# Optimization experiments

Hardware: AMD Instinct MI355X
Metric: run time of the kernel (lower is better)

## Reference

```python
import jax, jax.numpy as jnp
import numpy as np

HEAD_SIZE = 64
N_EMBD = 128
B, T = 16, 2048


def setup_inputs() -> dict:
    key = jax.random.key(0)
    ks = jax.random.split(key, 7)
    s = 1.0 / np.sqrt(N_EMBD)
    return {
        "x": jax.random.normal(ks[0], (B, T, N_EMBD), dtype=jnp.float32),
        "Wk": jax.random.normal(ks[1], (N_EMBD, HEAD_SIZE), dtype=jnp.float32) * s,
        "bk": jax.random.normal(ks[2], (HEAD_SIZE,), dtype=jnp.float32) * s,
        "Wq": jax.random.normal(ks[3], (N_EMBD, HEAD_SIZE), dtype=jnp.float32) * s,
        "bq": jax.random.normal(ks[4], (HEAD_SIZE,), dtype=jnp.float32) * s,
        "Wv": jax.random.normal(ks[5], (N_EMBD, HEAD_SIZE), dtype=jnp.float32) * s,
        "bv": jax.random.normal(ks[6], (HEAD_SIZE,), dtype=jnp.float32) * s,
    }


def reference(x, Wk, bk, Wq, bq, Wv, bv):
    # x: [B, T, C]; single-head causal attention (dropout in eval mode = identity)
    Tdim = x.shape[1]
    k = x @ Wk + bk  # [B, T, H]
    q = x @ Wq + bq  # [B, T, H]
    v = x @ Wv + bv  # [B, T, H]
    scale = jnp.asarray(k.shape[-1], x.dtype) ** -0.5
    wei = jnp.einsum("bth,bsh->bts", q, k) * scale  # [B, T, T]
    causal = jnp.tril(jnp.ones((Tdim, Tdim), dtype=bool))
    wei = jnp.where(causal, wei, -jnp.inf)
    wei = jax.nn.softmax(wei, axis=-1)
    out = jnp.einsum("bts,bsh->bth", wei, v)  # [B, T, H]
    return out
```

## Files before the change

kernel.cpp:

```cpp
#include <hip/hip_runtime.h>
#include <hip/hip_bf16.h>
#include <math.h>

#define HS 64
#define NE 128
#define TSEQ 2048

typedef short s8v __attribute__((ext_vector_type(8)));
typedef float f4v __attribute__((ext_vector_type(4)));

__device__ __forceinline__ unsigned short f2bf(float f) {
    unsigned int u = __float_as_uint(f);
    u += 0x7FFFu + ((u >> 16) & 1u);
    return (unsigned short)(u >> 16);
}

__device__ __forceinline__ unsigned int pkbf(float a, float b) {
    union { __hip_bfloat162 h; unsigned int u; } cv;
    cv.h = __float22bfloat162_rn(make_float2(a, b));
    return cv.u;
}

__device__ __forceinline__ s8v mk_s8v(unsigned int a, unsigned int b,
                                      unsigned int c, unsigned int d) {
    union { unsigned int u[4]; s8v v; } cv;
    cv.u[0] = a; cv.u[1] = b; cv.u[2] = c; cv.u[3] = d;
    return cv.v;
}

__device__ __forceinline__ float fexp2(float x) {
    float r;
    asm("v_exp_f32 %0, %1" : "=v"(r) : "v"(x));
    return r;
}

__device__ __forceinline__ void glds16(const unsigned short* g, unsigned short* l) {
    __builtin_amdgcn_global_load_lds(
        (const __attribute__((address_space(1))) unsigned int*)g,
        (__attribute__((address_space(3))) unsigned int*)l,
        16, 0, 0);
}

__global__ __launch_bounds__(256) void wconv(
    const float* __restrict__ Wq, const float* __restrict__ Wk,
    const float* __restrict__ Wv, unsigned short* __restrict__ wt)
{
    const int o0 = (blockIdx.x * 256 + threadIdx.x) * 2;
    const int mat = o0 >> 13;
    const int n = (o0 >> 7) & 63;
    const int k = o0 & 127;
    const float* W = (mat == 0) ? Wq : (mat == 1) ? Wk : Wv;
    const float s = (mat == 0) ? 0.18033688f : 1.0f;
    unsigned int lo = f2bf(W[k * HS + n] * s);
    unsigned int hi = f2bf(W[(k + 1) * HS + n] * s);
    *(unsigned int*)(wt + o0) = lo | (hi << 16);
}

__global__ __launch_bounds__(256) void qkv(
    const float* __restrict__ x, const unsigned short* __restrict__ wt,
    const float* __restrict__ bq, const float* __restrict__ bk,
    const float* __restrict__ bv,
    unsigned short* __restrict__ qo, unsigned short* __restrict__ ko,
    unsigned short* __restrict__ vt)
{
    __shared__ __align__(16) unsigned short Ws[192 * 136];

    const int tid = threadIdx.x;
    const int w = tid >> 6;
    const int lane = tid & 63;
    const int quad = lane >> 4;
    const int li = lane & 15;
    const size_t blk0 = (size_t)blockIdx.x * 64;
    const size_t row0w = blk0 + (size_t)w * 16;

#pragma unroll
    for (int p = 0; p < 12; ++p) {
        const int idx = p * 256 + tid;
        const int n = idx >> 4;
        const int c = idx & 15;
        s8v d = *(const s8v*)(wt + idx * 8);
        *(s8v*)&Ws[n * 136 + c * 8] = d;
    }

    s8v a[4];
    const float* xr = x + (row0w + li) * NE + quad * 8;
#pragma unroll
    for (int ks = 0; ks < 4; ++ks) {
        float4 f0 = *(const float4*)(xr + ks * 32);
        float4 f1 = *(const float4*)(xr + ks * 32 + 4);
        a[ks] = mk_s8v(pkbf(f0.x, f0.y), pkbf(f0.z, f0.w),
                       pkbf(f1.x, f1.y), pkbf(f1.z, f1.w));
    }

    __syncthreads();

    f4v acc[12];
#pragma unroll
    for (int nt = 0; nt < 12; ++nt) acc[nt] = (f4v){0.f, 0.f, 0.f, 0.f};

#pragma unroll
    for (int nt = 0; nt < 12; ++nt) {
        const unsigned short* wr = &Ws[(nt * 16 + li) * 136 + quad * 8];
#pragma unroll
        for (int ks = 0; ks < 4; ++ks) {
            s8v bfr = *(const s8v*)(wr + ks * 32);
            acc[nt] = __builtin_amdgcn_mfma_f32_16x16x32_bf16(a[ks], bfr, acc[nt], 0, 0, 0);
        }
    }

    const size_t bidx = row0w >> 11;
    const size_t trow0 = row0w & 2047;
#pragma unroll
    for (int nt = 0; nt < 4; ++nt) {
        const float bias = bv[nt * 16 + li];
        unsigned int lo = pkbf(acc[nt + 8][0] + bias, acc[nt + 8][1] + bias);
        unsigned int hi = pkbf(acc[nt + 8][2] + bias, acc[nt + 8][3] + bias);
        *(uint2*)(vt + (bidx * HS + nt * 16 + li) * TSEQ + trow0 + quad * 4) =
            make_uint2(lo, hi);
    }

    __syncthreads();

    float* Qt = (float*)Ws;
    float* Kt = Qt + 64 * 68;
    const float sq = 0.18033688f;
    const int lrow0 = w * 16 + quad * 4;
#pragma unroll
    for (int nt = 0; nt < 4; ++nt) {
        const int col = nt * 16 + li;
        const float bq_ = bq[col] * sq;
        const float bk_ = bk[col];
#pragma unroll
        for (int r = 0; r < 4; ++r) {
            Qt[(lrow0 + r) * 68 + col] = acc[nt][r] + bq_;
            Kt[(lrow0 + r) * 68 + col] = acc[nt + 4][r] + bk_;
        }
    }

    __syncthreads();

    const int row = tid >> 2;
    const int seg = tid & 3;
    {
        const float* src = &Qt[row * 68 + seg * 16];
        float4 f0 = *(const float4*)src;
        float4 f1 = *(const float4*)(src + 4);
        float4 f2 = *(const float4*)(src + 8);
        float4 f3 = *(const float4*)(src + 12);
        s8v d0 = mk_s8v(pkbf(f0.x, f0.y), pkbf(f0.z, f0.w), pkbf(f1.x, f1.y), pkbf(f1.z, f1.w));
        s8v d1 = mk_s8v(pkbf(f2.x, f2.y), pkbf(f2.z, f2.w), pkbf(f3.x, f3.y), pkbf(f3.z, f3.w));
        unsigned short* dst = qo + (blk0 + row) * HS + seg * 16;
        *(s8v*)dst = d0;
        *(s8v*)(dst + 8) = d1;
    }
    {
        const float* src = &Kt[row * 68 + seg * 16];
        float4 f0 = *(const float4*)src;
        float4 f1 = *(const float4*)(src + 4);
        float4 f2 = *(const float4*)(src + 8);
        float4 f3 = *(const float4*)(src + 12);
        s8v d0 = mk_s8v(pkbf(f0.x, f0.y), pkbf(f0.z, f0.w), pkbf(f1.x, f1.y), pkbf(f1.z, f1.w));
        s8v d1 = mk_s8v(pkbf(f2.x, f2.y), pkbf(f2.z, f2.w), pkbf(f3.x, f3.y), pkbf(f3.z, f3.w));
        unsigned short* dst = ko + (blk0 + row) * HS + seg * 16;
        *(s8v*)dst = d0;
        *(s8v*)(dst + 8) = d1;
    }
}

__device__ __forceinline__ void attn_tile_group(
    const unsigned short* Kc, const unsigned short* Vc,
    char* pbse, int lane, int quad, int li, int swz0, int swz1,
    int tl, int dg, int qrow, s8v qf0, s8v qf1, f4v* c_o, float& lsum)
{
    float pr[4][4];
    float rs = 0.f;
#pragma unroll
    for (int kt = 0; kt < 4; ++kt) {
        const unsigned short* krow = Kc + (kt * 16 + li) * 64;
        s8v k0 = *(const s8v*)(krow + swz0);
        s8v k1 = *(const s8v*)(krow + swz1);
        f4v cst = (f4v){0.f, 0.f, 0.f, 0.f};
        __builtin_amdgcn_s_setprio(1);
        cst = __builtin_amdgcn_mfma_f32_16x16x32_bf16(k0, qf0, cst, 0, 0, 0);
        cst = __builtin_amdgcn_mfma_f32_16x16x32_bf16(k1, qf1, cst, 0, 0, 0);
        __builtin_amdgcn_s_setprio(0);
        if (tl == dg) {
            const int key0 = (tl << 6) + kt * 16 + quad * 4;
#pragma unroll
            for (int rr = 0; rr < 4; ++rr)
                if (key0 + rr > qrow) cst[rr] = -INFINITY;
        }
#pragma unroll
        for (int rr = 0; rr < 4; ++rr) {
            pr[kt][rr] = fexp2(cst[rr]);
            rs += pr[kt][rr];
        }
    }
    lsum += rs;

#pragma unroll
    for (int kt = 0; kt < 4; ++kt) {
        *(uint2*)(pbse + (kt * 2 + (quad >> 1)) * 256 + li * 16 + (quad & 1) * 8) =
            make_uint2(pkbf(pr[kt][0], pr[kt][1]), pkbf(pr[kt][2], pr[kt][3]));
    }
    s8v pf0 = *(const s8v*)(pbse + lane * 16);
    s8v pf1 = *(const s8v*)(pbse + 1024 + lane * 16);

#pragma unroll
    for (int f = 0; f < 4; ++f) {
        const unsigned short* vrow = Vc + (f * 16 + li) * 64;
        s8v v0 = *(const s8v*)(vrow + swz0);
        s8v v1 = *(const s8v*)(vrow + swz1);
        __builtin_amdgcn_s_setprio(1);
        c_o[f] = __builtin_amdgcn_mfma_f32_16x16x32_bf16(v0, pf0, c_o[f], 0, 0, 0);
        c_o[f] = __builtin_amdgcn_mfma_f32_16x16x32_bf16(v1, pf1, c_o[f], 0, 0, 0);
        __builtin_amdgcn_s_setprio(0);
    }
}

__global__ __launch_bounds__(256) void attn_main(
    const unsigned short* __restrict__ qbf,
    const unsigned short* __restrict__ kb,
    const unsigned short* __restrict__ vtb,
    float* __restrict__ out, float* __restrict__ pbuf, float* __restrict__ lsbuf)
{
    __shared__ unsigned short Ks[2][64 * 64];
    __shared__ unsigned short Vs[2][64 * 64];
    __shared__ __align__(16) unsigned short Ps[4][1024];

    const int tid = threadIdx.x;
    const int w = tid >> 6;
    const int lane = tid & 63;
    const int quad = lane >> 4;
    const int li = lane & 15;

    const int id = blockIdx.x;
    const int xcd = id & 7;
    const int j = id >> 3;
    const int b = xcd * 2 + (j >= 40);
    const int jj = (j >= 40) ? j - 40 : j;
    const int u = 39 - jj;
    int qb, c, nc;
    if (u < 4)       { qb = u;                    c = 0;             nc = 1; }
    else if (u < 12) { qb = 4 + ((u - 4) >> 1);   c = (u - 4) & 1;   nc = 2; }
    else if (u < 24) { qb = 8 + (u - 12) / 3;     c = (u - 12) % 3;  nc = 3; }
    else             { qb = 12 + ((u - 24) >> 2); c = (u - 24) & 3;  nc = 4; }
    const int tb = c * 8;
    const int ntile = 2 * qb + 2;
    const int te = (tb + 8 < ntile) ? tb + 8 : ntile;

    const size_t base = (size_t)b * TSEQ;
    const int t0 = qb << 7;
    const int qrow0 = t0 + w * 16 + li;
    const int qrow1 = qrow0 + 64;
    const int d0 = 2 * qb;
    const int d1 = 2 * qb + 1;

    const unsigned short* qrp0 = qbf + (base + qrow0) * HS + quad * 8;
    s8v qA0 = *(const s8v*)qrp0;
    s8v qA1 = *(const s8v*)(qrp0 + 32);
    const unsigned short* qrp1 = qrp0 + 64 * HS;
    s8v qB0 = *(const s8v*)qrp1;
    s8v qB1 = *(const s8v*)(qrp1 + 32);

    const int rA = w * 8 + (lane >> 3);
    const int csw = (lane & 7) ^ (rA & 7);
    const unsigned short* kgA = kb + (base + rA) * HS + csw * 8;
    const unsigned short* kgB = kgA + 32 * HS;
    const unsigned short* vgA = vtb + ((size_t)b * HS + rA) * TSEQ + csw * 8;
    const unsigned short* vgB = vgA + 32 * TSEQ;
    const int ldsA = w * 512 + lane * 8;
    const int ldsB = 2048 + w * 512 + lane * 8;

    glds16(kgA + (size_t)tb * 4096, &Ks[0][ldsA]);
    glds16(kgB + (size_t)tb * 4096, &Ks[0][ldsB]);
    glds16(vgA + (size_t)tb * 64,   &Vs[0][ldsA]);
    glds16(vgB + (size_t)tb * 64,   &Vs[0][ldsB]);

    f4v c_oA[4], c_oB[4];
#pragma unroll
    for (int f = 0; f < 4; ++f) {
        c_oA[f] = (f4v){0.f, 0.f, 0.f, 0.f};
        c_oB[f] = (f4v){0.f, 0.f, 0.f, 0.f};
    }
    float lsA = 0.f, lsB = 0.f;

    char* pbse = (char*)&Ps[w][0];
    const int swz0 = (quad ^ (li & 7)) * 8;
    const int swz1 = ((4 + quad) ^ (li & 7)) * 8;

    __syncthreads();

    for (int tl = tb; tl < te; ++tl) {
        const int bi = (tl - tb) & 1;
        if (tl + 1 < te) {
            const int nb = bi ^ 1;
            glds16(kgA + (size_t)(tl + 1) * 4096, &Ks[nb][ldsA]);
            glds16(kgB + (size_t)(tl + 1) * 4096, &Ks[nb][ldsB]);
            glds16(vgA + (size_t)(tl + 1) * 64,   &Vs[nb][ldsA]);
            glds16(vgB + (size_t)(tl + 1) * 64,   &Vs[nb][ldsB]);
        }
        const unsigned short* Kc = &Ks[bi][0];
        const unsigned short* Vc = &Vs[bi][0];

        if (tl <= d0)
            attn_tile_group(Kc, Vc, pbse, lane, quad, li, swz0, swz1,
                            tl, d0, qrow0, qA0, qA1, c_oA, lsA);
        attn_tile_group(Kc, Vc, pbse, lane, quad, li, swz0, swz1,
                        tl, d1, qrow1, qB0, qB1, c_oB, lsB);

        __syncthreads();
    }

    lsA += __shfl_xor(lsA, 16);
    lsA += __shfl_xor(lsA, 32);
    lsB += __shfl_xor(lsB, 16);
    lsB += __shfl_xor(lsB, 32);

    if (nc == 1) {
        const float invA = 1.0f / lsA;
        float* orowA = out + (base + qrow0) * HS + quad * 4;
#pragma unroll
        for (int f = 0; f < 4; ++f) {
            f4v res = c_oA[f];
            res[0] *= invA; res[1] *= invA; res[2] *= invA; res[3] *= invA;
            *(f4v*)(orowA + f * 16) = res;
        }
        const float invB = 1.0f / lsB;
        float* orowB = out + (base + qrow1) * HS + quad * 4;
#pragma unroll
        for (int f = 0; f < 4; ++f) {
            f4v res = c_oB[f];
            res[0] *= invB; res[1] *= invB; res[2] *= invB; res[3] *= invB;
            *(f4v*)(orowB + f * 16) = res;
        }
    } else {
        const int local = (qb < 8)  ? (qb - 4) * 2 + c
                        : (qb < 12) ? 8 + (qb - 8) * 3 + c
                                    : 20 + (qb - 12) * 4 + c;
        const int pidx = b * 36 + local;
        float* pc = pbuf + (size_t)pidx * 8192 + (w * 16 + li) * 64;
#pragma unroll
        for (int f = 0; f < 4; ++f)
            *(f4v*)(pc + f * 16 + quad * 4) = c_oA[f];
        float* pc1 = pc + 64 * 64;
#pragma unroll
        for (int f = 0; f < 4; ++f)
            *(f4v*)(pc1 + f * 16 + quad * 4) = c_oB[f];
        if (quad == 0) {
            lsbuf[(size_t)pidx * 128 + w * 16 + li] = lsA;
            lsbuf[(size_t)pidx * 128 + 64 + w * 16 + li] = lsB;
        }
    }
}

__global__ __launch_bounds__(256) void attn_reduce(
    const float* __restrict__ pbuf, const float* __restrict__ lsbuf,
    float* __restrict__ out)
{
    const int g = blockIdx.x;
    const int b = g / 12;
    const int r = g - b * 12;
    int qb, lbase, nc;
    if (r < 4)      { qb = 4 + r;        lbase = 2 * r;            nc = 2; }
    else if (r < 8) { qb = 8 + (r - 4);  lbase = 8 + 3 * (r - 4);  nc = 3; }
    else            { qb = 12 + (r - 8); lbase = 20 + 4 * (r - 8); nc = 4; }
    const int pidx0 = b * 36 + lbase;

    const int tid = threadIdx.x;
    const int row = tid >> 1;
    const int seg = tid & 1;

    float4 acc[8];
#pragma unroll
    for (int j = 0; j < 8; ++j) acc[j] = make_float4(0.f, 0.f, 0.f, 0.f);
    float ls = 0.f;

    for (int cc = 0; cc < nc; ++cc) {
        const float* pc = pbuf + (size_t)(pidx0 + cc) * 8192 + row * 64 + seg * 32;
#pragma unroll
        for (int j = 0; j < 8; ++j) {
            float4 v = *(const float4*)(pc + j * 4);
            acc[j].x += v.x; acc[j].y += v.y; acc[j].z += v.z; acc[j].w += v.w;
        }
        ls += lsbuf[(size_t)(pidx0 + cc) * 128 + row];
    }
    const float inv = 1.0f / ls;
    float* orow = out + ((size_t)b * TSEQ + (qb << 7) + row) * HS + seg * 32;
#pragma unroll
    for (int j = 0; j < 8; ++j) {
        *(float4*)(orow + j * 4) = make_float4(acc[j].x * inv, acc[j].y * inv,
                                               acc[j].z * inv, acc[j].w * inv);
    }
}

extern "C" void kernel_launch(void* const* d_in, const int* in_sizes, int n_in,
                              void* d_out, int out_size, void* d_ws, size_t ws_size,
                              hipStream_t stream) {
    const float* x  = (const float*)d_in[0];
    const float* Wk = (const float*)d_in[1];
    const float* bk = (const float*)d_in[2];
    const float* Wq = (const float*)d_in[3];
    const float* bq = (const float*)d_in[4];
    const float* Wv = (const float*)d_in[5];
    const float* bv = (const float*)d_in[6];
    float* outp = (float*)d_out;

    const size_t elems = (size_t)16 * TSEQ * HS;
    unsigned short* qbuf = (unsigned short*)d_ws;
    unsigned short* kbuf = qbuf + elems;
    unsigned short* vbuf = kbuf + elems;
    unsigned short* wtb  = vbuf + elems;
    float* pbuf  = (float*)(wtb + 32768);
    float* lsbuf = pbuf + (size_t)576 * 8192;

    wconv<<<48, 256, 0, stream>>>(Wq, Wk, Wv, wtb);
    qkv<<<512, 256, 0, stream>>>(x, wtb, bq, bk, bv, qbuf, kbuf, vbuf);
    attn_main<<<640, 256, 0, stream>>>(qbuf, kbuf, vbuf, outp, pbuf, lsbuf);
    attn_reduce<<<192, 256, 0, stream>>>(pbuf, lsbuf, outp);
}
```

Before: 115.7 us.

## Fuse split-K reduction into attention kernel via atomic last-block counter, store partials as bf16

```diff
diff --git a/kernel.cpp b/kernel.cpp
--- a/kernel.cpp
+++ b/kernel.cpp
@@ -13,6 +13,10 @@
     unsigned int u = __float_as_uint(f);
     u += 0x7FFFu + ((u >> 16) & 1u);
     return (unsigned short)(u >> 16);
+}
+
+__device__ __forceinline__ float bf2f(unsigned short h) {
+    return __uint_as_float(((unsigned int)h) << 16);
 }
 
 __device__ __forceinline__ unsigned int pkbf(float a, float b) {
@@ -43,8 +47,10 @@
 
 __global__ __launch_bounds__(256) void wconv(
     const float* __restrict__ Wq, const float* __restrict__ Wk,
-    const float* __restrict__ Wv, unsigned short* __restrict__ wt)
+    const float* __restrict__ Wv, unsigned short* __restrict__ wt,
+    int* __restrict__ cnt)
 {
+    if (blockIdx.x == 0 && threadIdx.x < 192) cnt[threadIdx.x] = 0;
     const int o0 = (blockIdx.x * 256 + threadIdx.x) * 2;
     const int mat = o0 >> 13;
     const int n = (o0 >> 7) & 63;
@@ -222,11 +228,13 @@
     const unsigned short* __restrict__ qbf,
     const unsigned short* __restrict__ kb,
     const unsigned short* __restrict__ vtb,
-    float* __restrict__ out, float* __restrict__ pbuf, float* __restrict__ lsbuf)
+    float* __restrict__ out, unsigned short* __restrict__ pbf,
+    float* __restrict__ lsbuf, int* __restrict__ cnt)
 {
     __shared__ unsigned short Ks[2][64 * 64];
     __shared__ unsigned short Vs[2][64 * 64];
     __shared__ __align__(16) unsigned short Ps[4][1024];
+    __shared__ int lastFlag;
 
     const int tid = threadIdx.x;
     const int w = tid >> 6;
@@ -334,63 +342,72 @@
             res[0] *= invB; res[1] *= invB; res[2] *= invB; res[3] *= invB;
             *(f4v*)(orowB + f * 16) = res;
         }
-    } else {
-        const int local = (qb < 8)  ? (qb - 4) * 2 + c
-                        : (qb < 12) ? 8 + (qb - 8) * 3 + c
-                                    : 20 + (qb - 12) * 4 + c;
-        const int pidx = b * 36 + local;
-        float* pc = pbuf + (size_t)pidx * 8192 + (w * 16 + li) * 64;
-#pragma unroll
-        for (int f = 0; f < 4; ++f)
-            *(f4v*)(pc + f * 16 + quad * 4) = c_oA[f];
-        float* pc1 = pc + 64 * 64;
-#pragma unroll
-        for (int f = 0; f < 4; ++f)
-            *(f4v*)(pc1 + f * 16 + quad * 4) = c_oB[f];
-        if (quad == 0) {
-            lsbuf[(size_t)pidx * 128 + w * 16 + li] = lsA;
-            lsbuf[(size_t)pidx * 128 + 64 + w * 16 + li] = lsB;
-        }
-    }
-}
-
-__global__ __launch_bounds__(256) void attn_reduce(
-    const float* __restrict__ pbuf, const float* __restrict__ lsbuf,
-    float* __restrict__ out)
-{
-    const int g = blockIdx.x;
-    const int b = g / 12;
-    const int r = g - b * 12;
-    int qb, lbase, nc;
-    if (r < 4)      { qb = 4 + r;        lbase = 2 * r;            nc = 2; }
-    else if (r < 8) { qb = 8 + (r - 4);  lbase = 8 + 3 * (r - 4);  nc = 3; }
-    else            { qb = 12 + (r - 8); lbase = 20 + 4 * (r - 8); nc = 4; }
-    const int pidx0 = b * 36 + lbase;
-
-    const int tid = threadIdx.x;
+        return;
+    }
+
+    const int local = (qb < 8)  ? (qb - 4) * 2 + c
+                    : (qb < 12) ? 8 + (qb - 8) * 3 + c
+                                : 20 + (qb - 12) * 4 + c;
+    const int pidx = b * 36 + local;
+    unsigned short* pc = pbf + (size_t)pidx * 8192 + (w * 16 + li) * 64;
+#pragma unroll
+    for (int f = 0; f < 4; ++f) {
+        *(uint2*)(pc + f * 16 + quad * 4) =
+            make_uint2(pkbf(c_oA[f][0], c_oA[f][1]), pkbf(c_oA[f][2], c_oA[f][3]));
+    }
+    unsigned short* pc1 = pc + 64 * 64;
+#pragma unroll
+    for (int f = 0; f < 4; ++f) {
+        *(uint2*)(pc1 + f * 16 + quad * 4) =
+            make_uint2(pkbf(c_oB[f][0], c_oB[f][1]), pkbf(c_oB[f][2], c_oB[f][3]));
+    }
+    if (quad == 0) {
+        lsbuf[(size_t)pidx * 128 + w * 16 + li] = lsA;
+        lsbuf[(size_t)pidx * 128 + 64 + w * 16 + li] = lsB;
+    }
+
+    __threadfence();
+    __syncthreads();
+    const int qgrp = b * 12 + (qb - 4);
+    if (tid == 0) {
+        int old = atomicAdd(&cnt[qgrp], 1);
+        lastFlag = (old == nc - 1);
+    }
+    __syncthreads();
+    if (!lastFlag) return;
+    __threadfence();
+
+    const int lb = (qb < 8)  ? (qb - 4) * 2
+                 : (qb < 12) ? 8 + (qb - 8) * 3
+                             : 20 + (qb - 12) * 4;
+    const int p0 = b * 36 + lb;
     const int row = tid >> 1;
     const int seg = tid & 1;
 
-    float4 acc[8];
-#pragma unroll
-    for (int j = 0; j < 8; ++j) acc[j] = make_float4(0.f, 0.f, 0.f, 0.f);
+    float acc[32];
+#pragma unroll
+    for (int k = 0; k < 32; ++k) acc[k] = 0.f;
     float ls = 0.f;
 
     for (int cc = 0; cc < nc; ++cc) {
-        const float* pc = pbuf + (size_t)(pidx0 + cc) * 8192 + row * 64 + seg * 32;
-#pragma unroll
-        for (int j = 0; j < 8; ++j) {
-            float4 v = *(const float4*)(pc + j * 4);
-            acc[j].x += v.x; acc[j].y += v.y; acc[j].z += v.z; acc[j].w += v.w;
-        }
-        ls += lsbuf[(size_t)(pidx0 + cc) * 128 + row];
+        const unsigned short* ps = pbf + (size_t)(p0 + cc) * 8192 + row * 64 + seg * 32;
+#pragma unroll
+        for (int jj2 = 0; jj2 < 4; ++jj2) {
+            s8v v = *(const s8v*)(ps + jj2 * 8);
+#pragma unroll
+            for (int e = 0; e < 8; ++e)
+                acc[jj2 * 8 + e] += bf2f((unsigned short)v[e]);
+        }
+        ls += lsbuf[(size_t)(p0 + cc) * 128 + row];
     }
     const float inv = 1.0f / ls;
-    float* orow = out + ((size_t)b * TSEQ + (qb << 7) + row) * HS + seg * 32;
-#pragma unroll
-    for (int j = 0; j < 8; ++j) {
-        *(float4*)(orow + j * 4) = make_float4(acc[j].x * inv, acc[j].y * inv,
-                                               acc[j].z * inv, acc[j].w * inv);
+    float* orow = out + (base + (qb << 7) + row) * HS + seg * 32;
+#pragma unroll
+    for (int jj2 = 0; jj2 < 8; ++jj2) {
+        *(float4*)(orow + jj2 * 4) = make_float4(acc[jj2 * 4] * inv,
+                                                 acc[jj2 * 4 + 1] * inv,
+                                                 acc[jj2 * 4 + 2] * inv,
+                                                 acc[jj2 * 4 + 3] * inv);
     }
 }
 
@@ -411,11 +428,11 @@
     unsigned short* kbuf = qbuf + elems;
     unsigned short* vbuf = kbuf + elems;
     unsigned short* wtb  = vbuf + elems;
-    float* pbuf  = (float*)(wtb + 32768);
-    float* lsbuf = pbuf + (size_t)576 * 8192;
-
-    wconv<<<48, 256, 0, stream>>>(Wq, Wk, Wv, wtb);
+    unsigned short* pbf  = wtb + 32768;
+    float* lsbuf = (float*)(pbf + (size_t)576 * 8192);
+    int* cnt = (int*)(lsbuf + 576 * 128);
+
+    wconv<<<48, 256, 0, stream>>>(Wq, Wk, Wv, wtb, cnt);
     qkv<<<512, 256, 0, stream>>>(x, wtb, bq, bk, bv, qbuf, kbuf, vbuf);
-    attn_main<<<640, 256, 0, stream>>>(qbuf, kbuf, vbuf, outp, pbuf, lsbuf);
-    attn_reduce<<<192, 256, 0, stream>>>(pbuf, lsbuf, outp);
-}
+    attn_main<<<640, 256, 0, stream>>>(qbuf, kbuf, vbuf, outp, pbf, lsbuf, cnt);
+}
```

Result: slower. 202.0 us (+74.6%).

## Split KV into 4-tile chunks with bf16 partial outputs for finer load balance

Applied to the files above, without the earlier changes.

```diff
diff --git a/kernel.cpp b/kernel.cpp
--- a/kernel.cpp
+++ b/kernel.cpp
@@ -13,6 +13,10 @@
     unsigned int u = __float_as_uint(f);
     u += 0x7FFFu + ((u >> 16) & 1u);
     return (unsigned short)(u >> 16);
+}
+
+__device__ __forceinline__ float bf2f(unsigned short h) {
+    return __uint_as_float(((unsigned int)h) << 16);
 }
 
 __device__ __forceinline__ unsigned int pkbf(float a, float b) {
@@ -222,7 +226,8 @@
     const unsigned short* __restrict__ qbf,
     const unsigned short* __restrict__ kb,
     const unsigned short* __restrict__ vtb,
-    float* __restrict__ out, float* __restrict__ pbuf, float* __restrict__ lsbuf)
+    float* __restrict__ out, unsigned short* __restrict__ pbf,
+    float* __restrict__ lsbuf)
 {
     __shared__ unsigned short Ks[2][64 * 64];
     __shared__ unsigned short Vs[2][64 * 64];
@@ -237,17 +242,19 @@
     const int id = blockIdx.x;
     const int xcd = id & 7;
     const int j = id >> 3;
-    const int b = xcd * 2 + (j >= 40);
-    const int jj = (j >= 40) ? j - 40 : j;
-    const int u = 39 - jj;
-    int qb, c, nc;
-    if (u < 4)       { qb = u;                    c = 0;             nc = 1; }
-    else if (u < 12) { qb = 4 + ((u - 4) >> 1);   c = (u - 4) & 1;   nc = 2; }
-    else if (u < 24) { qb = 8 + (u - 12) / 3;     c = (u - 12) % 3;  nc = 3; }
-    else             { qb = 12 + ((u - 24) >> 2); c = (u - 24) & 3;  nc = 4; }
-    const int tb = c * 8;
+    const int b = xcd * 2 + (j >= 72);
+    const int jj = (j >= 72) ? j - 72 : j;
+    const int u = 71 - jj;
+
+    int m = 0;
+    while ((m + 1) * (m + 2) <= u) ++m;
+    const int rem = u - m * (m + 1);
+    const int qb = 2 * m + (rem > m ? 1 : 0);
+    const int c = (rem > m) ? rem - (m + 1) : rem;
+    const int nc = m + 1;
+    const int tb = c * 4;
     const int ntile = 2 * qb + 2;
-    const int te = (tb + 8 < ntile) ? tb + 8 : ntile;
+    const int te = (tb + 4 < ntile) ? tb + 4 : ntile;
 
     const size_t base = (size_t)b * TSEQ;
     const int t0 = qb << 7;
@@ -335,18 +342,19 @@
             *(f4v*)(orowB + f * 16) = res;
         }
     } else {
-        const int local = (qb < 8)  ? (qb - 4) * 2 + c
-                        : (qb < 12) ? 8 + (qb - 8) * 3 + c
-                                    : 20 + (qb - 12) * 4 + c;
-        const int pidx = b * 36 + local;
-        float* pc = pbuf + (size_t)pidx * 8192 + (w * 16 + li) * 64;
-#pragma unroll
-        for (int f = 0; f < 4; ++f)
-            *(f4v*)(pc + f * 16 + quad * 4) = c_oA[f];
-        float* pc1 = pc + 64 * 64;
-#pragma unroll
-        for (int f = 0; f < 4; ++f)
-            *(f4v*)(pc1 + f * 16 + quad * 4) = c_oB[f];
+        const int pidx = b * 70 + (u - 2);
+        unsigned short* pc = pbf + (size_t)pidx * 8192 + (w * 16 + li) * 64;
+#pragma unroll
+        for (int f = 0; f < 4; ++f) {
+            *(uint2*)(pc + f * 16 + quad * 4) =
+                make_uint2(pkbf(c_oA[f][0], c_oA[f][1]), pkbf(c_oA[f][2], c_oA[f][3]));
+        }
+        unsigned short* pc1 = pc + 64 * 64;
+#pragma unroll
+        for (int f = 0; f < 4; ++f) {
+            *(uint2*)(pc1 + f * 16 + quad * 4) =
+                make_uint2(pkbf(c_oB[f][0], c_oB[f][1]), pkbf(c_oB[f][2], c_oB[f][3]));
+        }
         if (quad == 0) {
             lsbuf[(size_t)pidx * 128 + w * 16 + li] = lsA;
             lsbuf[(size_t)pidx * 128 + 64 + w * 16 + li] = lsB;
@@ -355,42 +363,46 @@
 }
 
 __global__ __launch_bounds__(256) void attn_reduce(
-    const float* __restrict__ pbuf, const float* __restrict__ lsbuf,
+    const unsigned short* __restrict__ pbf, const float* __restrict__ lsbuf,
     float* __restrict__ out)
 {
     const int g = blockIdx.x;
-    const int b = g / 12;
-    const int r = g - b * 12;
-    int qb, lbase, nc;
-    if (r < 4)      { qb = 4 + r;        lbase = 2 * r;            nc = 2; }
-    else if (r < 8) { qb = 8 + (r - 4);  lbase = 8 + 3 * (r - 4);  nc = 3; }
-    else            { qb = 12 + (r - 8); lbase = 20 + 4 * (r - 8); nc = 4; }
-    const int pidx0 = b * 36 + lbase;
+    const int b = g / 28;
+    const int rem = g - b * 28;
+    const int r = 2 + (rem >> 1);
+    const int half = rem & 1;
+    const int m = r >> 1;
+    const int nc = m + 1;
+    const int pidx0 = b * 70 + m * (m + 1) + (r & 1) * (m + 1) - 2;
 
     const int tid = threadIdx.x;
-    const int row = tid >> 1;
-    const int seg = tid & 1;
-
-    float4 acc[8];
-#pragma unroll
-    for (int j = 0; j < 8; ++j) acc[j] = make_float4(0.f, 0.f, 0.f, 0.f);
+    const int row = half * 64 + (tid >> 2);
+    const int seg = tid & 3;
+
+    float acc[16];
+#pragma unroll
+    for (int k = 0; k < 16; ++k) acc[k] = 0.f;
     float ls = 0.f;
 
     for (int cc = 0; cc < nc; ++cc) {
-        const float* pc = pbuf + (size_t)(pidx0 + cc) * 8192 + row * 64 + seg * 32;
-#pragma unroll
-        for (int j = 0; j < 8; ++j) {
-            float4 v = *(const float4*)(pc + j * 4);
-            acc[j].x += v.x; acc[j].y += v.y; acc[j].z += v.z; acc[j].w += v.w;
+        const unsigned short* ps = pbf + (size_t)(pidx0 + cc) * 8192 + row * 64 + seg * 16;
+        s8v v0 = *(const s8v*)ps;
+        s8v v1 = *(const s8v*)(ps + 8);
+#pragma unroll
+        for (int e = 0; e < 8; ++e) {
+            acc[e] += bf2f((unsigned short)v0[e]);
+            acc[8 + e] += bf2f((unsigned short)v1[e]);
         }
         ls += lsbuf[(size_t)(pidx0 + cc) * 128 + row];
     }
     const float inv = 1.0f / ls;
-    float* orow = out + ((size_t)b * TSEQ + (qb << 7) + row) * HS + seg * 32;
-#pragma unroll
-    for (int j = 0; j < 8; ++j) {
-        *(float4*)(orow + j * 4) = make_float4(acc[j].x * inv, acc[j].y * inv,
-                                               acc[j].z * inv, acc[j].w * inv);
+    float* orow = out + ((size_t)b * TSEQ + (r << 7) + row) * HS + seg * 16;
+#pragma unroll
+    for (int jj = 0; jj < 4; ++jj) {
+        *(float4*)(orow + jj * 4) = make_float4(acc[jj * 4] * inv,
+                                                acc[jj * 4 + 1] * inv,
+                                                acc[jj * 4 + 2] * inv,
+                                                acc[jj * 4 + 3] * inv);
     }
 }
 
@@ -411,11 +423,11 @@
     unsigned short* kbuf = qbuf + elems;
     unsigned short* vbuf = kbuf + elems;
     unsigned short* wtb  = vbuf + elems;
-    float* pbuf  = (float*)(wtb + 32768);
-    float* lsbuf = pbuf + (size_t)576 * 8192;
+    unsigned short* pbf  = wtb + 32768;
+    float* lsbuf = (float*)(pbf + (size_t)1120 * 8192);
 
     wconv<<<48, 256, 0, stream>>>(Wq, Wk, Wv, wtb);
     qkv<<<512, 256, 0, stream>>>(x, wtb, bq, bk, bv, qbuf, kbuf, vbuf);
-    attn_main<<<640, 256, 0, stream>>>(qbuf, kbuf, vbuf, outp, pbuf, lsbuf);
-    attn_reduce<<<192, 256, 0, stream>>>(pbuf, lsbuf, outp);
-}
+    attn_main<<<1152, 256, 0, stream>>>(qbuf, kbuf, vbuf, outp, pbf, lsbuf);
+    attn_reduce<<<448, 256, 0, stream>>>(pbf, lsbuf, outp);
+}
```

New measurement: 114.3 us. Within noise of the previous version (-1.2%).
